# Optimization experiments

Measured on AMD Instinct MI355X. Metric: run time of the kernel, lower is better.

## Reference

```python
import jax, jax.numpy as jnp
import numpy as np

H = 2048
MAX_DEPTH = 2
BASIS = 4


def setup_inputs() -> dict:
    key = jax.random.key(0)
    ks = jax.random.split(key, 16)
    s = 0.02

    def w(k, shape):
        return jax.random.normal(k, shape, dtype=jnp.float32) * s

    return dict(
        x=jax.random.normal(ks[0], (1, H), dtype=jnp.float32),
        h=jax.random.normal(ks[1], (1, H), dtype=jnp.float32),
        c=jax.random.normal(ks[2], (1, H), dtype=jnp.float32),
        Wq=w(ks[3], (H, H)), Wk=w(ks[4], (H, H)), Wv=w(ks[5], (H, H)), Wo=w(ks[6], (H, H)),
        Wih=w(ks[7], (H, 4 * H)), Whh=w(ks[8], (H, 4 * H)),
        b_lstm=jnp.zeros((4 * H,), jnp.float32),
        router_w=w(ks[9], (H, BASIS)), router_b=jnp.zeros((BASIS,), jnp.float32),
        expert_w=w(ks[10], (BASIS, H, H)), expert_b=jnp.zeros((BASIS, H), jnp.float32),
        dr_w=w(ks[11], (H, MAX_DEPTH + 1)),
        # bias the depth router toward the deepest choice so the recursion tree is exercised
        dr_b=jnp.array([0.0, 1.0, 5.0], jnp.float32),
        ram_w=w(ks[12], (2 * H, H)), ram_b=jnp.zeros((H,), jnp.float32),
        ag_w=w(ks[13], (2 * H, H)), ag_b=jnp.zeros((H,), jnp.float32),
    )


def reference(x, h, c, Wq, Wk, Wv, Wo, Wih, Whh, b_lstm, router_w, router_b,
              expert_w, expert_b, dr_w, dr_b, ram_w, ram_b, ag_w, ag_b):
    def cell_step(x_, h_, c_):
        # Single-token multi-head attention: softmax over a length-1 axis is
        # identically 1, so attention collapses to (h @ Wv) @ Wo; Wq/Wk are
        # parameters with zero effective gradient (matches torch behavior).
        attn = (h_ @ Wv) @ Wo
        gates = x_ @ Wih + attn @ Whh + b_lstm  # [1, 4H]
        i, f, g, o = jnp.split(gates, 4, axis=1)
        c2 = jax.nn.sigmoid(f) * c_ + jax.nn.sigmoid(i) * jnp.tanh(g)
        h2 = jax.nn.sigmoid(o) * jnp.tanh(c2)
        return h2, h2, c2

    def path_gate(hh):
        p = jax.nn.softmax(hh @ router_w + router_b, axis=1)          # [1, E]
        eo = jnp.einsum('bh,ehk->bek', hh, expert_w) + expert_b        # [1, E, H]
        return jnp.einsum('be,bek->bk', p, eo)                         # [1, H]

    def ramanujan(states):
        # alternating-harmonic (Ramanujan-summation style) weighted reduction
        agg = states[0] * 0.0
        for n, s in enumerate(states):
            agg = agg + (((-1.0) ** n) / (n + 1)) * s
        return jnp.concatenate([agg, states[0]], axis=1) @ ram_w + ram_b

    def fwd(x_, h_, c_, depth):
        so, hs, cs = cell_step(x_, h_, c_)
        hp = path_gate(hs)
        # mirrors torch.no_grad() + .item() host sync
        chosen = int(jnp.argmax(hp @ dr_w + dr_b, axis=1)[0])
        steps = min(chosen, max(0, MAX_DEPTH - depth))
        if steps <= 0:
            return so, hp, cs
        h_cur, c_cur, final = hp, cs, so
        states = [h_cur]
        for _ in range(steps):
            damping = 1.0 / (depth + 1) ** 2
            ro, hnr, cn = fwd(x_, h_cur, c_cur, depth + 1)
            h_next = h_cur + damping * (hnr - h_cur)  # torch.lerp
            states.append(h_next)
            h_cur, c_cur, final = h_next, cn, ro
        anchor = ramanujan(states)
        g = jax.nn.sigmoid(jnp.concatenate([h_cur, anchor], axis=1) @ ag_w + ag_b)
        return final, g * anchor + (1.0 - g) * h_cur, c_cur

    return fwd(x, h, c, 0)
```

## Files before the change

### kernel.cpp

```cpp
#include <hip/hip_runtime.h>
#include <math.h>


#define H 2048
#define NB 512

struct P {
  const float *x, *h0, *c0, *Wv, *Wo, *Wih, *Whh, *b_lstm, *router_w, *router_b,
              *expert_w, *expert_b, *dr_w, *dr_b, *ram_w, *ram_b, *ag_w, *ag_b;
  float* out;
  float* ws;
};

constexpr int CTRU   = 2048;
constexpr int DL     = 2048;
constexpr int GT     = 2064;
constexpr int NODE   = 10256;
constexpr int NODESZ = 26624;
constexpr int THV = 0, ATT = 2048, GAC = 4096, EO = 12288, SO = 20480, CS = 22528, HP = 24576;
constexpr int FIN    = NODE + 5 * NODESZ;
constexpr int FINSZ  = 8192;
constexpr int ANC = 0, GCC = 2048, HNo = 4096, AGGo = 6144;
constexpr int RH1 = FIN + 3 * FINSZ;
constexpr int RF1 = RH1 + 2048;
constexpr int RC1 = RH1 + 4096;
constexpr int ZTOT = 5 * 20480 + 3 * 4096;

__device__ __forceinline__ float sigm(float v) { return 1.f / (1.f + expf(-v)); }

__device__ __forceinline__ float coh_f(const float* p) {
  return __hip_atomic_load(p, __ATOMIC_RELAXED, __HIP_MEMORY_SCOPE_AGENT);
}
__device__ __forceinline__ void coh_st(float* p, float v) {
  __hip_atomic_store(p, v, __ATOMIC_RELAXED, __HIP_MEMORY_SCOPE_AGENT);
}

__device__ __forceinline__ int dsteps(const float* dla, const float* drb, int mx) {
  const float l0 = dla[0] + drb[0], l1 = dla[1] + drb[1], l2 = dla[2] + drb[2];
  int ch = 0; float bv = l0;
  if (l1 > bv) { bv = l1; ch = 1; }
  if (l2 > bv) { bv = l2; ch = 2; }
  return ch < mx ? ch : mx;
}

__device__ __forceinline__ bool pred(const float* ws, const float* drb, int code) {
  if (code == 0) return true;
  const int s0 = dsteps(ws + DL, drb, 2);
  switch (code) {
    case 1: return s0 >= 1;
    case 2: return s0 >= 1 && dsteps(ws + DL + 4, drb, 1) >= 1;
    case 3: return s0 >= 2;
    case 4: return s0 >= 2 && dsteps(ws + DL + 8, drb, 1) >= 1;
  }
  return true;
}

__device__ __forceinline__ void resbar(unsigned* ctr, int phase) {
  asm volatile("s_waitcnt vmcnt(0)" ::: "memory");
  __syncthreads();
  if (threadIdx.x == 0) {
    unsigned* sub = ctr + (blockIdx.x & 7) * 16;
    unsigned* master = ctr + 128;
    const unsigned prev = __hip_atomic_fetch_add(sub, 1u, __ATOMIC_RELAXED, __HIP_MEMORY_SCOPE_AGENT);
    if (prev == (unsigned)(64 * phase) - 1u)
      __hip_atomic_fetch_add(master, 1u, __ATOMIC_RELAXED, __HIP_MEMORY_SCOPE_AGENT);
    long t = 0;
    while (__hip_atomic_load(master, __ATOMIC_RELAXED, __HIP_MEMORY_SCOPE_AGENT) <
           (unsigned)(8 * phase)) {
      __builtin_amdgcn_s_sleep(8);
      if (++t > 20000000L) break;
    }
  }
  __syncthreads();
}

template <int CHUNK, int XMODE>
__device__ __forceinline__ void gemv_phase(
    int bid, int G,
    const float* xA, const float* xB, int splitPt, const float* xBias,
    const float* __restrict__ W, float* __restrict__ y, int N,
    float* shx, float4* red)
{
  const int tid = threadIdx.x, lane = tid & 63, tsub = tid >> 6;
  const int g = bid % G, s = bid / G;
  const int base = s * CHUNK;
  for (int idx = tid; idx < CHUNK; idx += 256) {
    const int i = base + idx;
    float v;
    if (XMODE == 0)      v = (i < splitPt) ? xA[i] : xB[i - splitPt];
    else if (XMODE == 1) v = coh_f(xA + i);
    else                 v = (i < splitPt) ? xA[i] : (xBias[i - splitPt] + coh_f(xB + (i - splitPt)));
    shx[idx] = v;
  }
  __syncthreads();
  constexpr int LEN = CHUNK / 4;
  const int j = (g << 8) + (lane << 2);
  const float* Wp = W + (size_t)(base + tsub * LEN) * N + j;
  float ax = 0.f, ay = 0.f, az = 0.f, aw = 0.f;
#pragma unroll
  for (int t = 0; t < LEN; ++t) {
    const float xi = shx[tsub * LEN + t];
    const float4 wv = *reinterpret_cast<const float4*>(Wp + (size_t)t * N);
    ax = fmaf(xi, wv.x, ax); ay = fmaf(xi, wv.y, ay);
    az = fmaf(xi, wv.z, az); aw = fmaf(xi, wv.w, aw);
  }
  red[tid] = make_float4(ax, ay, az, aw);
  __syncthreads();
  if (tsub == 0) {
    float4 a = red[tid], b = red[tid + 64], c = red[tid + 128], d = red[tid + 192];
    atomicAdd(&y[j + 0], a.x + b.x + c.x + d.x);
    atomicAdd(&y[j + 1], a.y + b.y + c.y + d.y);
    atomicAdd(&y[j + 2], a.z + b.z + c.z + d.z);
    atomicAdd(&y[j + 3], a.w + b.w + c.w + d.w);
  }
}

__device__ void expert_phase(const P& p, float* nb, const float* c_in, const float* gt,
                             float* shx, float4* red)
{
  const int tid = threadIdx.x, lane = tid & 63, w = tid >> 6;
  const int g = blockIdx.x & 31, s = blockIdx.x >> 5;
  const int i0 = s * 128;
  if (tid < 128) {
    const int i = i0 + tid;
    const float gi = p.b_lstm[i]         + coh_f(gt + i)         + coh_f(nb + GAC + i);
    const float gf = p.b_lstm[H + i]     + coh_f(gt + H + i)     + coh_f(nb + GAC + H + i);
    const float gg = p.b_lstm[2 * H + i] + coh_f(gt + 2 * H + i) + coh_f(nb + GAC + 2 * H + i);
    const float go = p.b_lstm[3 * H + i] + coh_f(gt + 3 * H + i) + coh_f(nb + GAC + 3 * H + i);
    const float c2 = sigm(gf) * c_in[i] + sigm(gi) * tanhf(gg);
    const float h2 = sigm(go) * tanhf(c2);
    shx[tid] = h2;
    if (g == 0) { coh_st(nb + SO + i, h2); coh_st(nb + CS + i, c2); }
  }
  __syncthreads();
  const int j = (g << 8) + (lane << 2);
  const int e = j >> 11, k = j & (H - 1);
  const float* Wp = p.expert_w + ((size_t)e << 22) + (size_t)(i0 + w * 32) * H + k;
  float ax = 0.f, ay = 0.f, az = 0.f, aw = 0.f;
#pragma unroll
  for (int t = 0; t < 32; ++t) {
    const float xi = shx[w * 32 + t];
    const float4 wv = *reinterpret_cast<const float4*>(Wp + (size_t)t * H);
    ax = fmaf(xi, wv.x, ax); ay = fmaf(xi, wv.y, ay);
    az = fmaf(xi, wv.z, az); aw = fmaf(xi, wv.w, aw);
  }
  red[tid] = make_float4(ax, ay, az, aw);
  __syncthreads();
  if (w == 0) {
    float4 a = red[tid], b = red[tid + 64], c = red[tid + 128], d = red[tid + 192];
    atomicAdd(&nb[EO + j + 0], a.x + b.x + c.x + d.x);
    atomicAdd(&nb[EO + j + 1], a.y + b.y + c.y + d.y);
    atomicAdd(&nb[EO + j + 2], a.z + b.z + c.z + d.z);
    atomicAdd(&nb[EO + j + 3], a.w + b.w + c.w + d.w);
  }
}

__device__ void combine_phase(const P& p, float* nb, float* dla, int leaf, float damping,
                              const float* php, float* hn, float* agg, float4* red)
{
  const int tid = threadIdx.x;
  float r0 = 0.f, r1 = 0.f, r2 = 0.f, r3 = 0.f;
  for (int i = tid; i < H; i += 256) {
    const float hh = coh_f(nb + SO + i);
    const float4 rw = *reinterpret_cast<const float4*>(p.router_w + i * 4);
    r0 = fmaf(hh, rw.x, r0); r1 = fmaf(hh, rw.y, r1);
    r2 = fmaf(hh, rw.z, r2); r3 = fmaf(hh, rw.w, r3);
  }
  red[tid] = make_float4(r0, r1, r2, r3);
  __syncthreads();
  for (int off = 128; off > 0; off >>= 1) {
    if (tid < off) {
      const float4 b = red[tid + off];
      red[tid].x += b.x; red[tid].y += b.y; red[tid].z += b.z; red[tid].w += b.w;
    }
    __syncthreads();
  }
  const float4 L = red[0];
  __syncthreads();
  const float l0 = L.x + p.router_b[0], l1 = L.y + p.router_b[1];
  const float l2 = L.z + p.router_b[2], l3 = L.w + p.router_b[3];
  const float m = fmaxf(fmaxf(l0, l1), fmaxf(l2, l3));
  const float e0 = expf(l0 - m), e1 = expf(l1 - m), e2 = expf(l2 - m), e3 = expf(l3 - m);
  const float inv = 1.f / (e0 + e1 + e2 + e3);
  const float q0 = e0 * inv, q1 = e1 * inv, q2 = e2 * inv, q3 = e3 * inv;
  const int jj = blockIdx.x * 256 + tid;
  const float v = q0 * (p.expert_b[jj]         + coh_f(nb + EO + jj))
                + q1 * (p.expert_b[H + jj]     + coh_f(nb + EO + H + jj))
                + q2 * (p.expert_b[2 * H + jj] + coh_f(nb + EO + 2 * H + jj))
                + q3 * (p.expert_b[3 * H + jj] + coh_f(nb + EO + 3 * H + jj));
  if (leaf) {
    const float h0v = php[jj];
    const float hnv = h0v + damping * (v - h0v);
    hn[jj] = hnv;
    agg[jj] = h0v - 0.5f * hnv;
  } else {
    nb[HP + jj] = v;
    red[tid] = make_float4(v * p.dr_w[jj * 3 + 0], v * p.dr_w[jj * 3 + 1], v * p.dr_w[jj * 3 + 2], 0.f);
    __syncthreads();
    for (int off = 128; off > 0; off >>= 1) {
      if (tid < off) {
        const float4 b = red[tid + off];
        red[tid].x += b.x; red[tid].y += b.y; red[tid].z += b.z;
      }
      __syncthreads();
    }
    if (tid == 0) {
      atomicAdd(&dla[0], red[0].x);
      atomicAdd(&dla[1], red[0].y);
      atomicAdd(&dla[2], red[0].z);
    }
  }
}

__device__ void tail_fsel(const P& p, float* ws) {
  if (dsteps(ws + DL, p.dr_b, 2) < 1) return;
  const bool deep = dsteps(ws + DL + 4, p.dr_b, 1) >= 1;
  const int jj = blockIdx.x * 256 + threadIdx.x;
  const float* n1 = ws + NODE + 1 * NODESZ;
  const float* n2 = ws + NODE + 2 * NODESZ;
  const float* fb = ws + FIN;
  float rh, rf, rc;
  if (deep) {
    const float gacc = p.ag_b[jj] + coh_f(fb + GCC + jj);
    const float anc  = p.ram_b[jj] + coh_f(fb + ANC + jj);
    const float g = sigm(gacc);
    rh = g * anc + (1.f - g) * fb[HNo + jj];
    rf = n2[SO + jj]; rc = n2[CS + jj];
  } else {
    rh = n1[HP + jj]; rf = n1[SO + jj]; rc = n1[CS + jj];
  }
  ws[RH1 + jj] = rh; ws[RF1 + jj] = rf; ws[RC1 + jj] = rc;
}

__device__ void tail1(const P& p, float* ws) {
  const int s0 = dsteps(ws + DL, p.dr_b, 2);
  if (s0 < 1) return;
  const int jj = blockIdx.x * 256 + threadIdx.x;
  const float* n0 = ws + NODE;
  const float* n3 = ws + NODE + 3 * NODESZ;
  const float* n4 = ws + NODE + 4 * NODESZ;
  const float* fb3 = ws + FIN + FINSZ;
  float* fb0 = ws + FIN + 2 * FINSZ;
  const float r1 = ws[RH1 + jj];
  float rh3 = 0.f, rf3 = 0.f, rc3 = 0.f;
  if (s0 >= 2) {
    if (dsteps(ws + DL + 8, p.dr_b, 1) >= 1) {
      const float gacc = p.ag_b[jj] + coh_f(fb3 + GCC + jj);
      const float anc  = p.ram_b[jj] + coh_f(fb3 + ANC + jj);
      const float g = sigm(gacc);
      rh3 = g * anc + (1.f - g) * fb3[HNo + jj];
      rf3 = n4[SO + jj]; rc3 = n4[CS + jj];
    } else { rh3 = n3[HP + jj]; rf3 = n3[SO + jj]; rc3 = n3[CS + jj]; }
  }
  float ag = n0[HP + jj] - 0.5f * r1;
  float hc, oF, oC;
  if (s0 >= 2) { ag += (1.f / 3.f) * rh3; hc = rh3; oF = rf3; oC = rc3; }
  else { hc = r1; oF = ws[RF1 + jj]; oC = ws[RC1 + jj]; }
  fb0[AGGo + jj] = ag; fb0[HNo + jj] = hc;
  p.out[jj] = oF; p.out[2 * H + jj] = oC;
}

__device__ void tail2(const P& p, float* ws) {
  const int s0 = dsteps(ws + DL, p.dr_b, 2);
  const int jj = blockIdx.x * 256 + threadIdx.x;
  const float* n0 = ws + NODE;
  const float* fb0 = ws + FIN + 2 * FINSZ;
  if (s0 == 0) {
    p.out[jj] = n0[SO + jj]; p.out[H + jj] = n0[HP + jj]; p.out[2 * H + jj] = n0[CS + jj];
  } else {
    const float gacc = p.ag_b[jj] + coh_f(fb0 + GCC + jj);
    const float anc  = p.ram_b[jj] + coh_f(fb0 + ANC + jj);
    const float g = sigm(gacc);
    p.out[H + jj] = g * anc + (1.f - g) * fb0[HNo + jj];
  }
}

__global__ void __launch_bounds__(256) k_zero(P p) {
  float* ws = p.ws;
  const int gtid = blockIdx.x * 256 + threadIdx.x;
  const int gsz = gridDim.x * 256;
  unsigned* u = (unsigned*)ws;
  for (int i = gtid; i < CTRU; i += gsz) u[i] = 0u;
  if (gtid < 12) ws[DL + gtid] = 0.f;
  for (int i = gtid; i < 8192; i += gsz) ws[GT + i] = 0.f;
}

__global__ void __launch_bounds__(256, 2) k_prep(P p) {
  float* ws = p.ws;
  __shared__ float shx[128];
  __shared__ float4 red[256];
  const int gtid = blockIdx.x * 256 + threadIdx.x;
  for (int i = gtid; i < ZTOT; i += NB * 256) {
    if (i < 5 * 20480) {
      const int n = i / 20480, off = i % 20480;
      ws[NODE + n * NODESZ + off] = 0.f;
    } else {
      const int j = i - 5 * 20480;
      ws[FIN + (j >> 12) * FINSZ + (j & 4095)] = 0.f;
    }
  }
  gemv_phase<128, 0>(blockIdx.x, 32, p.x, p.x, 1 << 30, nullptr, p.Wih, ws + GT, 4 * H, shx, red);
}

__global__ void __launch_bounds__(256, 2) k_node(
    P p, int nodeIdx, int ctrIdx, int predCode,
    const float* hv, const float* cv,
    int leaf, float damping, const float* php, float* hn, float* agg, float* dla)
{
  float* ws = p.ws;
  if (!pred(ws, p.dr_b, predCode)) return;
  __shared__ float shx[128];
  __shared__ float4 red[256];
  float* nb = ws + NODE + nodeIdx * NODESZ;
  unsigned* ctr = (unsigned*)ws + ctrIdx * 256;
  gemv_phase<32, 0>(blockIdx.x, 8, hv, hv, 1 << 30, nullptr, p.Wv, nb + THV, H, shx, red);
  resbar(ctr, 1);
  gemv_phase<32, 1>(blockIdx.x, 8, nb + THV, nullptr, 0, nullptr, p.Wo, nb + ATT, H, shx, red);
  resbar(ctr, 2);
  gemv_phase<128, 1>(blockIdx.x, 32, nb + ATT, nullptr, 0, nullptr, p.Whh, nb + GAC, 4 * H, shx, red);
  resbar(ctr, 3);
  expert_phase(p, nb, cv, ws + GT, shx, red);
  resbar(ctr, 4);
  if (blockIdx.x >= 8) return;
  combine_phase(p, nb, dla, leaf, damping, php, hn, agg, red);
}

__global__ void __launch_bounds__(256, 2) k_fin(
    P p, int finIdx, int ctrIdx, int predCode,
    const float* aggv, const float* phpv, const float* hnv, int tailKind)
{
  float* ws = p.ws;
  __shared__ float shx[64];
  __shared__ float4 red[256];
  float* fb = ws + FIN + finIdx * FINSZ;
  unsigned* ctr = (unsigned*)ws + ctrIdx * 256;
  const bool ok = pred(ws, p.dr_b, predCode);
  if (ok) {
    gemv_phase<64, 0>(blockIdx.x, 8, aggv, phpv, H, nullptr, p.ram_w, fb + ANC, H, shx, red);
    resbar(ctr, 1);
    gemv_phase<64, 2>(blockIdx.x, 8, hnv, fb + ANC, H, p.ram_b, p.ag_w, fb + GCC, H, shx, red);
    resbar(ctr, 2);
  }
  if (blockIdx.x >= 8) return;
  if (tailKind == 1) tail_fsel(p, ws);
  else if (tailKind == 2) tail1(p, ws);
  else tail2(p, ws);
}

extern "C" void kernel_launch(void* const* d_in, const int* in_sizes, int n_in,
                              void* d_out, int out_size, void* d_ws, size_t ws_size,
                              hipStream_t stream) {
  P p;
  p.x = (const float*)d_in[0];  p.h0 = (const float*)d_in[1];  p.c0 = (const float*)d_in[2];
  p.Wv = (const float*)d_in[5]; p.Wo = (const float*)d_in[6];
  p.Wih = (const float*)d_in[7]; p.Whh = (const float*)d_in[8];
  p.b_lstm = (const float*)d_in[9];
  p.router_w = (const float*)d_in[10]; p.router_b = (const float*)d_in[11];
  p.expert_w = (const float*)d_in[12]; p.expert_b = (const float*)d_in[13];
  p.dr_w = (const float*)d_in[14]; p.dr_b = (const float*)d_in[15];
  p.ram_w = (const float*)d_in[16]; p.ram_b = (const float*)d_in[17];
  p.ag_w = (const float*)d_in[18]; p.ag_b = (const float*)d_in[19];
  p.out = (float*)d_out;
  p.ws = (float*)d_ws;

  float* ws = p.ws;
  auto nb = [&](int n) { return ws + NODE + n * NODESZ; };
  float* fb1 = ws + FIN;
  float* fb3 = ws + FIN + FINSZ;
  float* fb0 = ws + FIN + 2 * FINSZ;

  k_zero<<<8, 256, 0, stream>>>(p);
  k_prep<<<NB, 256, 0, stream>>>(p);
  k_node<<<NB, 256, 0, stream>>>(p, 0, 0, 0, p.h0, p.c0,
                                 0, 0.f, nullptr, nullptr, nullptr, ws + DL);
  k_node<<<NB, 256, 0, stream>>>(p, 1, 1, 1, nb(0) + HP, nb(0) + CS,
                                 0, 0.f, nullptr, nullptr, nullptr, ws + DL + 4);
  k_node<<<NB, 256, 0, stream>>>(p, 2, 2, 2, nb(1) + HP, nb(1) + CS,
                                 1, 0.25f, nb(1) + HP, fb1 + HNo, fb1 + AGGo, nullptr);
  k_fin<<<NB, 256, 0, stream>>>(p, 0, 3, 2, fb1 + AGGo, nb(1) + HP, fb1 + HNo, 1);
  k_node<<<NB, 256, 0, stream>>>(p, 3, 4, 3, ws + RH1, ws + RC1,
                                 0, 0.f, nullptr, nullptr, nullptr, ws + DL + 8);
  k_node<<<NB, 256, 0, stream>>>(p, 4, 5, 4, nb(3) + HP, nb(3) + CS,
                                 1, 0.25f, nb(3) + HP, fb3 + HNo, fb3 + AGGo, nullptr);
  k_fin<<<NB, 256, 0, stream>>>(p, 1, 6, 4, fb3 + AGGo, nb(3) + HP, fb3 + HNo, 2);
  k_fin<<<NB, 256, 0, stream>>>(p, 2, 7, 1, fb0 + AGGo, nb(0) + HP, fb0 + HNo, 3);
}
```

Measured before the change: 378.2 us.

## Replace atomicAdd GEMV reductions with per-slice partial buffers reduced by consumers

Each GEMV split-K slice now writes its partial output vector to a dedicated buffer slot with plain coherent stores instead of atomically adding into a shared accumulator. The next phase sums the 16 or 64 partials while loading its input, and the combine, expert and tail stages sum the partial slices too. This removes the atomic contention and the workspace zeroing passes in k_zero and k_prep. In exchange the workspace grows greatly and consumers do many more coherent loads, up to 64 per element.

```diff
diff --git a/kernel.cpp b/kernel.cpp
--- a/kernel.cpp
+++ b/kernel.cpp
@@ -14,17 +14,22 @@
 
 constexpr int CTRU   = 2048;
 constexpr int DL     = 2048;
-constexpr int GT     = 2064;
-constexpr int NODE   = 10256;
-constexpr int NODESZ = 26624;
-constexpr int THV = 0, ATT = 2048, GAC = 4096, EO = 12288, SO = 20480, CS = 22528, HP = 24576;
+constexpr int GTP    = 2064;
+constexpr int NODE   = 133136;
+constexpr int NODESZ = 530432;
+constexpr int THVP = 0;
+constexpr int ATTP = 131072;
+constexpr int GACP = 262144;
+constexpr int EOP  = 393216;
+constexpr int SO = 524288, CS = 526336, HP = 528384;
 constexpr int FIN    = NODE + 5 * NODESZ;
-constexpr int FINSZ  = 8192;
-constexpr int ANC = 0, GCC = 2048, HNo = 4096, AGGo = 6144;
+constexpr int FINSZ  = 268288;
+constexpr int ANCP = 0;
+constexpr int GCCP = 131072;
+constexpr int ANCF = 262144, HNo = 264192, AGGo = 266240;
 constexpr int RH1 = FIN + 3 * FINSZ;
 constexpr int RF1 = RH1 + 2048;
 constexpr int RC1 = RH1 + 4096;
-constexpr int ZTOT = 5 * 20480 + 3 * 4096;
 
 __device__ __forceinline__ float sigm(float v) { return 1.f / (1.f + expf(-v)); }
 
@@ -74,25 +79,51 @@
   __syncthreads();
 }
 
-template <int CHUNK, int XMODE>
+template <int CHUNK, int KS_IN, int XMODE>
 __device__ __forceinline__ void gemv_phase(
     int bid, int G,
     const float* xA, const float* xB, int splitPt, const float* xBias,
-    const float* __restrict__ W, float* __restrict__ y, int N,
-    float* shx, float4* red)
+    const float* xpart, int pw,
+    const float* __restrict__ W, float* ypart, int N,
+    float* emitBuf, float* shx, float4* red)
 {
   const int tid = threadIdx.x, lane = tid & 63, tsub = tid >> 6;
   const int g = bid % G, s = bid / G;
   const int base = s * CHUNK;
-  for (int idx = tid; idx < CHUNK; idx += 256) {
-    const int i = base + idx;
-    float v;
-    if (XMODE == 0)      v = (i < splitPt) ? xA[i] : xB[i - splitPt];
-    else if (XMODE == 1) v = coh_f(xA + i);
-    else                 v = (i < splitPt) ? xA[i] : (xBias[i - splitPt] + coh_f(xB + (i - splitPt)));
-    shx[idx] = v;
-  }
-  __syncthreads();
+  constexpr int GRP = 256 / CHUNK;
+  const int elem = tid & (CHUNK - 1);
+  const int sg = tid / CHUNK;
+  float* scr = (float*)red;
+  {
+    const int i = base + elem;
+    float acc = 0.f;
+    if (XMODE == 0) {
+      if (sg == 0) acc = (i < splitPt) ? xA[i] : xB[i - splitPt];
+    } else if (XMODE == 1) {
+      for (int ss = sg; ss < KS_IN; ss += GRP) acc += coh_f(xpart + ss * pw + i);
+    } else {
+      if (i < splitPt) {
+        if (sg == 0) acc = xA[i];
+      } else {
+        const int ii = i - splitPt;
+        if (sg == 0) acc = xBias[ii];
+        for (int ss = sg; ss < KS_IN; ss += GRP) acc += coh_f(xpart + ss * pw + ii);
+      }
+    }
+    scr[tid] = acc;
+  }
+  __syncthreads();
+  if (tid < CHUNK) {
+    float v = 0.f;
+#pragma unroll
+    for (int k = 0; k < GRP; ++k) v += scr[k * CHUNK + tid];
+    shx[tid] = v;
+  }
+  __syncthreads();
+  if (emitBuf && g == 0 && tid < CHUNK) {
+    const int i = base + tid;
+    if (i >= splitPt) coh_st(emitBuf + (i - splitPt), shx[tid]);
+  }
   constexpr int LEN = CHUNK / 4;
   const int j = (g << 8) + (lane << 2);
   const float* Wp = W + (size_t)(base + tsub * LEN) * N + j;
@@ -108,27 +139,35 @@
   __syncthreads();
   if (tsub == 0) {
     float4 a = red[tid], b = red[tid + 64], c = red[tid + 128], d = red[tid + 192];
-    atomicAdd(&y[j + 0], a.x + b.x + c.x + d.x);
-    atomicAdd(&y[j + 1], a.y + b.y + c.y + d.y);
-    atomicAdd(&y[j + 2], a.z + b.z + c.z + d.z);
-    atomicAdd(&y[j + 3], a.w + b.w + c.w + d.w);
-  }
-}
-
-__device__ void expert_phase(const P& p, float* nb, const float* c_in, const float* gt,
-                             float* shx, float4* red)
+    float* yp = ypart + (size_t)s * N + j;
+    coh_st(yp + 0, a.x + b.x + c.x + d.x);
+    coh_st(yp + 1, a.y + b.y + c.y + d.y);
+    coh_st(yp + 2, a.z + b.z + c.z + d.z);
+    coh_st(yp + 3, a.w + b.w + c.w + d.w);
+  }
+  __syncthreads();
+}
+
+__device__ void expert_phase(const P& p, float* nb, const float* c_in,
+                             const float* gtp, float* shx, float4* red)
 {
   const int tid = threadIdx.x, lane = tid & 63, w = tid >> 6;
   const int g = blockIdx.x & 31, s = blockIdx.x >> 5;
   const int i0 = s * 128;
   if (tid < 128) {
     const int i = i0 + tid;
-    const float gi = p.b_lstm[i]         + coh_f(gt + i)         + coh_f(nb + GAC + i);
-    const float gf = p.b_lstm[H + i]     + coh_f(gt + H + i)     + coh_f(nb + GAC + H + i);
-    const float gg = p.b_lstm[2 * H + i] + coh_f(gt + 2 * H + i) + coh_f(nb + GAC + 2 * H + i);
-    const float go = p.b_lstm[3 * H + i] + coh_f(gt + 3 * H + i) + coh_f(nb + GAC + 3 * H + i);
-    const float c2 = sigm(gf) * c_in[i] + sigm(gi) * tanhf(gg);
-    const float h2 = sigm(go) * tanhf(c2);
+    float gv[4];
+#pragma unroll
+    for (int q = 0; q < 4; ++q) {
+      float a = p.b_lstm[q * H + i];
+#pragma unroll
+      for (int ss = 0; ss < 16; ++ss) a += coh_f(gtp + ss * 8192 + q * H + i);
+#pragma unroll
+      for (int ss = 0; ss < 16; ++ss) a += coh_f(nb + GACP + ss * 8192 + q * H + i);
+      gv[q] = a;
+    }
+    const float c2 = sigm(gv[1]) * c_in[i] + sigm(gv[0]) * tanhf(gv[2]);
+    const float h2 = sigm(gv[3]) * tanhf(c2);
     shx[tid] = h2;
     if (g == 0) { coh_st(nb + SO + i, h2); coh_st(nb + CS + i, c2); }
   }
@@ -148,17 +187,28 @@
   __syncthreads();
   if (w == 0) {
     float4 a = red[tid], b = red[tid + 64], c = red[tid + 128], d = red[tid + 192];
-    atomicAdd(&nb[EO + j + 0], a.x + b.x + c.x + d.x);
-    atomicAdd(&nb[EO + j + 1], a.y + b.y + c.y + d.y);
-    atomicAdd(&nb[EO + j + 2], a.z + b.z + c.z + d.z);
-    atomicAdd(&nb[EO + j + 3], a.w + b.w + c.w + d.w);
-  }
+    float* yp = nb + EOP + (size_t)s * 8192 + j;
+    coh_st(yp + 0, a.x + b.x + c.x + d.x);
+    coh_st(yp + 1, a.y + b.y + c.y + d.y);
+    coh_st(yp + 2, a.z + b.z + c.z + d.z);
+    coh_st(yp + 3, a.w + b.w + c.w + d.w);
+  }
+  __syncthreads();
 }
 
 __device__ void combine_phase(const P& p, float* nb, float* dla, int leaf, float damping,
                               const float* php, float* hn, float* agg, float4* red)
 {
   const int tid = threadIdx.x;
+  const int jj = blockIdx.x * 256 + tid;
+  float eo0 = p.expert_b[jj], eo1 = p.expert_b[H + jj],
+        eo2 = p.expert_b[2 * H + jj], eo3 = p.expert_b[3 * H + jj];
+#pragma unroll
+  for (int ss = 0; ss < 16; ++ss) {
+    const float* ep = nb + EOP + ss * 8192;
+    eo0 += coh_f(ep + jj); eo1 += coh_f(ep + H + jj);
+    eo2 += coh_f(ep + 2 * H + jj); eo3 += coh_f(ep + 3 * H + jj);
+  }
   float r0 = 0.f, r1 = 0.f, r2 = 0.f, r3 = 0.f;
   for (int i = tid; i < H; i += 256) {
     const float hh = coh_f(nb + SO + i);
@@ -182,12 +232,7 @@
   const float m = fmaxf(fmaxf(l0, l1), fmaxf(l2, l3));
   const float e0 = expf(l0 - m), e1 = expf(l1 - m), e2 = expf(l2 - m), e3 = expf(l3 - m);
   const float inv = 1.f / (e0 + e1 + e2 + e3);
-  const float q0 = e0 * inv, q1 = e1 * inv, q2 = e2 * inv, q3 = e3 * inv;
-  const int jj = blockIdx.x * 256 + tid;
-  const float v = q0 * (p.expert_b[jj]         + coh_f(nb + EO + jj))
-                + q1 * (p.expert_b[H + jj]     + coh_f(nb + EO + H + jj))
-                + q2 * (p.expert_b[2 * H + jj] + coh_f(nb + EO + 2 * H + jj))
-                + q3 * (p.expert_b[3 * H + jj] + coh_f(nb + EO + 3 * H + jj));
+  const float v = (e0 * eo0 + e1 * eo1 + e2 * eo2 + e3 * eo3) * inv;
   if (leaf) {
     const float h0v = php[jj];
     const float hnv = h0v + damping * (v - h0v);
@@ -212,6 +257,15 @@
   }
 }
 
+__device__ __forceinline__ float gated_mix(const P& p, const float* fb, int jj, float hnv) {
+  float gacc = p.ag_b[jj];
+#pragma unroll
+  for (int ss = 0; ss < 64; ++ss) gacc += coh_f(fb + GCCP + ss * 2048 + jj);
+  const float anc = coh_f(fb + ANCF + jj);
+  const float g = sigm(gacc);
+  return g * anc + (1.f - g) * hnv;
+}
+
 __device__ void tail_fsel(const P& p, float* ws) {
   if (dsteps(ws + DL, p.dr_b, 2) < 1) return;
   const bool deep = dsteps(ws + DL + 4, p.dr_b, 1) >= 1;
@@ -221,10 +275,7 @@
   const float* fb = ws + FIN;
   float rh, rf, rc;
   if (deep) {
-    const float gacc = p.ag_b[jj] + coh_f(fb + GCC + jj);
-    const float anc  = p.ram_b[jj] + coh_f(fb + ANC + jj);
-    const float g = sigm(gacc);
-    rh = g * anc + (1.f - g) * fb[HNo + jj];
+    rh = gated_mix(p, fb, jj, fb[HNo + jj]);
     rf = n2[SO + jj]; rc = n2[CS + jj];
   } else {
     rh = n1[HP + jj]; rf = n1[SO + jj]; rc = n1[CS + jj];
@@ -245,10 +296,7 @@
   float rh3 = 0.f, rf3 = 0.f, rc3 = 0.f;
   if (s0 >= 2) {
     if (dsteps(ws + DL + 8, p.dr_b, 1) >= 1) {
-      const float gacc = p.ag_b[jj] + coh_f(fb3 + GCC + jj);
-      const float anc  = p.ram_b[jj] + coh_f(fb3 + ANC + jj);
-      const float g = sigm(gacc);
-      rh3 = g * anc + (1.f - g) * fb3[HNo + jj];
+      rh3 = gated_mix(p, fb3, jj, fb3[HNo + jj]);
       rf3 = n4[SO + jj]; rc3 = n4[CS + jj];
     } else { rh3 = n3[HP + jj]; rf3 = n3[SO + jj]; rc3 = n3[CS + jj]; }
   }
@@ -268,38 +316,22 @@
   if (s0 == 0) {
     p.out[jj] = n0[SO + jj]; p.out[H + jj] = n0[HP + jj]; p.out[2 * H + jj] = n0[CS + jj];
   } else {
-    const float gacc = p.ag_b[jj] + coh_f(fb0 + GCC + jj);
-    const float anc  = p.ram_b[jj] + coh_f(fb0 + ANC + jj);
-    const float g = sigm(gacc);
-    p.out[H + jj] = g * anc + (1.f - g) * fb0[HNo + jj];
+    p.out[H + jj] = gated_mix(p, fb0, jj, fb0[HNo + jj]);
   }
 }
 
 __global__ void __launch_bounds__(256) k_zero(P p) {
   float* ws = p.ws;
   const int gtid = blockIdx.x * 256 + threadIdx.x;
-  const int gsz = gridDim.x * 256;
-  unsigned* u = (unsigned*)ws;
-  for (int i = gtid; i < CTRU; i += gsz) u[i] = 0u;
+  if (gtid < CTRU) ((unsigned*)ws)[gtid] = 0u;
   if (gtid < 12) ws[DL + gtid] = 0.f;
-  for (int i = gtid; i < 8192; i += gsz) ws[GT + i] = 0.f;
 }
 
 __global__ void __launch_bounds__(256, 2) k_prep(P p) {
-  float* ws = p.ws;
   __shared__ float shx[128];
   __shared__ float4 red[256];
-  const int gtid = blockIdx.x * 256 + threadIdx.x;
-  for (int i = gtid; i < ZTOT; i += NB * 256) {
-    if (i < 5 * 20480) {
-      const int n = i / 20480, off = i % 20480;
-      ws[NODE + n * NODESZ + off] = 0.f;
-    } else {
-      const int j = i - 5 * 20480;
-      ws[FIN + (j >> 12) * FINSZ + (j & 4095)] = 0.f;
-    }
-  }
-  gemv_phase<128, 0>(blockIdx.x, 32, p.x, p.x, 1 << 30, nullptr, p.Wih, ws + GT, 4 * H, shx, red);
+  gemv_phase<128, 0, 0>(blockIdx.x, 32, p.x, p.x, 1 << 30, nullptr, nullptr, 0,
+                        p.Wih, p.ws + GTP, 4 * H, nullptr, shx, red);
 }
 
 __global__ void __launch_bounds__(256, 2) k_node(
@@ -313,13 +345,16 @@
   __shared__ float4 red[256];
   float* nb = ws + NODE + nodeIdx * NODESZ;
   unsigned* ctr = (unsigned*)ws + ctrIdx * 256;
-  gemv_phase<32, 0>(blockIdx.x, 8, hv, hv, 1 << 30, nullptr, p.Wv, nb + THV, H, shx, red);
+  gemv_phase<32, 0, 0>(blockIdx.x, 8, hv, hv, 1 << 30, nullptr, nullptr, 0,
+                       p.Wv, nb + THVP, H, nullptr, shx, red);
   resbar(ctr, 1);
-  gemv_phase<32, 1>(blockIdx.x, 8, nb + THV, nullptr, 0, nullptr, p.Wo, nb + ATT, H, shx, red);
+  gemv_phase<32, 64, 1>(blockIdx.x, 8, nullptr, nullptr, 0, nullptr, nb + THVP, 2048,
+                        p.Wo, nb + ATTP, H, nullptr, shx, red);
   resbar(ctr, 2);
-  gemv_phase<128, 1>(blockIdx.x, 32, nb + ATT, nullptr, 0, nullptr, p.Whh, nb + GAC, 4 * H, shx, red);
+  gemv_phase<128, 64, 1>(blockIdx.x, 32, nullptr, nullptr, 0, nullptr, nb + ATTP, 2048,
+                         p.Whh, nb + GACP, 4 * H, nullptr, shx, red);
   resbar(ctr, 3);
-  expert_phase(p, nb, cv, ws + GT, shx, red);
+  expert_phase(p, nb, cv, ws + GTP, shx, red);
   resbar(ctr, 4);
   if (blockIdx.x >= 8) return;
   combine_phase(p, nb, dla, leaf, damping, php, hn, agg, red);
@@ -330,15 +365,17 @@
     const float* aggv, const float* phpv, const float* hnv, int tailKind)
 {
   float* ws = p.ws;
-  __shared__ float shx[64];
+  __shared__ float shx[128];
   __shared__ float4 red[256];
   float* fb = ws + FIN + finIdx * FINSZ;
   unsigned* ctr = (unsigned*)ws + ctrIdx * 256;
   const bool ok = pred(ws, p.dr_b, predCode);
   if (ok) {
-    gemv_phase<64, 0>(blockIdx.x, 8, aggv, phpv, H, nullptr, p.ram_w, fb + ANC, H, shx, red);
+    gemv_phase<64, 0, 0>(blockIdx.x, 8, aggv, phpv, H, nullptr, nullptr, 0,
+                         p.ram_w, fb + ANCP, H, nullptr, shx, red);
     resbar(ctr, 1);
-    gemv_phase<64, 2>(blockIdx.x, 8, hnv, fb + ANC, H, p.ram_b, p.ag_w, fb + GCC, H, shx, red);
+    gemv_phase<64, 64, 2>(blockIdx.x, 8, hnv, nullptr, H, p.ram_b, fb + ANCP, 2048,
+                          p.ag_w, fb + GCCP, H, fb + ANCF, shx, red);
     resbar(ctr, 2);
   }
   if (blockIdx.x >= 8) return;
```

Measured after the change: 438.3 us. 1.16x slower.
